# Kernel tuning notes

Measured on AMD Instinct MI355X. Metric: run time of the kernel, lower is better.

The kernel has to match this reference:

```python
import jax, jax.numpy as jnp
import numpy as np

EMB = 64
N_CONS = 100000
N_VARS = 200000
N_EDGES = 2000000


def _embed(x, shift, scale, W1, b1, W2, b2):
    # PreNormLayer (affine) -> Linear -> ReLU -> Linear -> ReLU
    x = (x - shift) * scale
    x = jax.nn.relu(x @ W1 + b1)
    return jax.nn.relu(x @ W2 + b2)


def _biconv(left, right, ei0, ei1, edge_lin, tgt_idx, n_tgt, tgt_feats,
            Wl, bl, Wr, sf, Wf, bf, sp, Woa, boa, Wob, bob):
    # gather-transform: per-edge joint features [E, EMB]
    joint = (left @ Wl + bl)[ei0] + edge_lin + (right @ Wr)[ei1]
    # feature_module_final: PreNorm(scale-only) -> ReLU -> Linear
    msg = jax.nn.relu(joint * sf) @ Wf + bf
    # scatter-add to target nodes, then post-conv PreNorm(scale-only)
    agg = jax.ops.segment_sum(msg, tgt_idx, num_segments=n_tgt) * sp
    h = jax.nn.relu(jnp.concatenate([agg, tgt_feats], axis=1) @ Woa + boa)
    return h @ Wob + bob


def _forward(constraint_features, edge_features, variable_features,
             c_shift, c_scale, c_W1, c_b1, c_W2, c_b2,
             v_shift, v_scale, v_W1, v_b1, v_W2, v_b2,
             e_shift, e_scale,
             vc_Wl, vc_bl, vc_We, vc_Wr, vc_sf, vc_Wf, vc_bf, vc_sp,
             vc_Woa, vc_boa, vc_Wob, vc_bob,
             cv_Wl, cv_bl, cv_We, cv_Wr, cv_sf, cv_Wf, cv_bf, cv_sp,
             cv_Woa, cv_boa, cv_Wob, cv_bob,
             out_W1, out_b1, out_W2, edge_indices):
    ei0, ei1 = edge_indices[0], edge_indices[1]
    c = _embed(constraint_features, c_shift, c_scale, c_W1, c_b1, c_W2, c_b2)
    v = _embed(variable_features, v_shift, v_scale, v_W1, v_b1, v_W2, v_b2)
    e = (edge_features - e_shift) * e_scale  # edge embedding = PreNorm only, dim 1
    # conv_v_to_c (right_to_left=True): target = constraints via ei0
    c = jax.nn.relu(_biconv(c, v, ei0, ei1, e @ vc_We, ei0, N_CONS, c,
                            vc_Wl, vc_bl, vc_Wr, vc_sf, vc_Wf, vc_bf, vc_sp,
                            vc_Woa, vc_boa, vc_Wob, vc_bob))
    # conv_c_to_v: target = variables via ei1
    v = jax.nn.relu(_biconv(c, v, ei0, ei1, e @ cv_We, ei1, N_VARS, v,
                            cv_Wl, cv_bl, cv_Wr, cv_sf, cv_Wf, cv_bf, cv_sp,
                            cv_Woa, cv_boa, cv_Wob, cv_bob))
    out = jax.nn.relu(v @ out_W1 + out_b1) @ out_W2  # [N_VARS, 1]
    return out.reshape(1, -1)


def setup_inputs():
    key = jax.random.key(0)
    ks = iter(jax.random.split(key, 64))

    def rn(shape, s=0.1):
        return (jax.random.normal(next(ks), shape, jnp.float32) * s).astype(jnp.float32)

    d = {}
    d["constraint_features"] = rn((N_CONS, 5), 1.0)
    d["edge_features"] = rn((N_EDGES, 1), 1.0)
    d["variable_features"] = rn((N_VARS, 19), 1.0)

    def prenorm(n, pre):
        d[pre + "shift"] = rn((n,), 0.05)
        d[pre + "scale"] = jnp.ones((n,), jnp.float32) + rn((n,), 0.05)

    prenorm(5, "c_"); prenorm(19, "v_"); prenorm(1, "e_")
    for pre, nin in (("c_", 5), ("v_", 19)):
        d[pre + "W1"] = rn((nin, EMB)); d[pre + "b1"] = rn((EMB,), 0.02)
        d[pre + "W2"] = rn((EMB, EMB)); d[pre + "b2"] = rn((EMB,), 0.02)
    for pre in ("vc_", "cv_"):
        d[pre + "Wl"] = rn((EMB, EMB)); d[pre + "bl"] = rn((EMB,), 0.02)
        d[pre + "We"] = rn((1, EMB)); d[pre + "Wr"] = rn((EMB, EMB))
        d[pre + "sf"] = jnp.float32(1.0) + rn((), 0.05)
        d[pre + "Wf"] = rn((EMB, EMB)); d[pre + "bf"] = rn((EMB,), 0.02)
        d[pre + "sp"] = jnp.float32(1.0) + rn((), 0.05)
        d[pre + "Woa"] = rn((2 * EMB, EMB)); d[pre + "boa"] = rn((EMB,), 0.02)
        d[pre + "Wob"] = rn((EMB, EMB)); d[pre + "bob"] = rn((EMB,), 0.02)
    d["out_W1"] = rn((EMB, EMB)); d["out_b1"] = rn((EMB,), 0.02)
    d["out_W2"] = rn((EMB, 1))
    d["edge_indices"] = jnp.stack([
        jax.random.randint(next(ks), (N_EDGES,), 0, N_CONS),
        jax.random.randint(next(ks), (N_EDGES,), 0, N_VARS)]).astype(jnp.int32)
    d["n_cons_per_sample"] = jnp.array([N_CONS], jnp.int32)
    d["n_vars_per_sample"] = jnp.array([N_VARS], jnp.int32)
    return d


def reference(constraint_features, edge_features, variable_features,
              c_shift, c_scale, c_W1, c_b1, c_W2, c_b2,
              v_shift, v_scale, v_W1, v_b1, v_W2, v_b2,
              e_shift, e_scale,
              vc_Wl, vc_bl, vc_We, vc_Wr, vc_sf, vc_Wf, vc_bf, vc_sp,
              vc_Woa, vc_boa, vc_Wob, vc_bob,
              cv_Wl, cv_bl, cv_We, cv_Wr, cv_sf, cv_Wf, cv_bf, cv_sp,
              cv_Woa, cv_boa, cv_Wob, cv_bob,
              out_W1, out_b1, out_W2,
              edge_indices, n_cons_per_sample, n_vars_per_sample):
    return _forward(constraint_features, edge_features, variable_features,
                    c_shift, c_scale, c_W1, c_b1, c_W2, c_b2,
                    v_shift, v_scale, v_W1, v_b1, v_W2, v_b2,
                    e_shift, e_scale,
                    vc_Wl, vc_bl, vc_We, vc_Wr, vc_sf, vc_Wf, vc_bf, vc_sp,
                    vc_Woa, vc_boa, vc_Wob, vc_bob,
                    cv_Wl, cv_bl, cv_We, cv_Wr, cv_sf, cv_Wf, cv_bf, cv_sp,
                    cv_Woa, cv_boa, cv_Wob, cv_bob,
                    out_W1, out_b1, out_W2, edge_indices)
```

## Files before the change

### kernel.cpp

```cpp
#include <hip/hip_runtime.h>
#include <hip/hip_bf16.h>

#define DEV __device__ __forceinline__

typedef __attribute__((ext_vector_type(8))) short short8;
typedef __attribute__((ext_vector_type(4))) float f32x4;

DEV unsigned short f2bf(float f) {
    __hip_bfloat16 h = __float2bfloat16(f);
    unsigned short u;
    __builtin_memcpy(&u, &h, 2);
    return u;
}
DEV float bf2f(unsigned short u) { return __uint_as_float((unsigned int)u << 16); }

DEV f32x4 mfma_bf16(short8 a, short8 b, f32x4 c) {
    return __builtin_amdgcn_mfma_f32_16x16x32_bf16(a, b, c, 0, 0, 0);
}

DEV void make_hilo(const float* a8, short8& hi, short8& lo) {
    #pragma unroll
    for (int j = 0; j < 8; ++j) {
        const float v = a8[j];
        const unsigned short h = f2bf(v);
        hi[j] = (short)h;
        lo[j] = (short)f2bf(v - bf2f(h));
    }
}

DEV void mfma3(f32x4 acc[4], short8 ah, short8 al,
               const unsigned short* __restrict__ Bh,
               const unsigned short* __restrict__ Bl,
               int nkt, int tidx, int lane) {
    #pragma unroll
    for (int c = 0; c < 4; ++c) {
        const size_t o = ((size_t)(c * nkt + tidx) * 64 + lane) * 8;
        const short8 bh = *(const short8*)(Bh + o);
        const short8 bl = *(const short8*)(Bl + o);
        acc[c] = mfma_bf16(ah, bh, acc[c]);
        acc[c] = mfma_bf16(al, bh, acc[c]);
        acc[c] = mfma_bf16(ah, bl, acc[c]);
    }
}

DEV int swf(int row, int col) {
    return row * 64 + ((((col >> 3) ^ row) & 7) << 3) + (col & 7);
}

DEV void gemm_lds(f32x4 acc[4], const float* Xl,
                  const unsigned short* Bh, const unsigned short* Bl,
                  int nkt, int t0, int ntk, int l15, int q, int lane) {
    for (int t = 0; t < ntk; ++t) {
        const int ch = (t * 4 + q) ^ (l15 & 7);
        const float* a8 = Xl + l15 * 64 + ch * 8;
        short8 ah, al;
        make_hilo(a8, ah, al);
        mfma3(acc, ah, al, Bh, Bl, nkt, t0 + t, lane);
    }
}

DEV void gemm_glb(f32x4 acc[4], const float* __restrict__ Xg, int rbase, int N,
                  const unsigned short* Bh, const unsigned short* Bl,
                  int nkt, int t0, int ntk, int l15, int q, int lane) {
    const int grow = rbase + l15;
    const bool ok = grow < N;
    for (int t = 0; t < ntk; ++t) {
        float a8[8];
        if (ok) {
            const float4 v0 = *(const float4*)(Xg + (size_t)grow * 64 + t * 32 + q * 8);
            const float4 v1 = *(const float4*)(Xg + (size_t)grow * 64 + t * 32 + q * 8 + 4);
            a8[0] = v0.x; a8[1] = v0.y; a8[2] = v0.z; a8[3] = v0.w;
            a8[4] = v1.x; a8[5] = v1.y; a8[6] = v1.z; a8[7] = v1.w;
        } else {
            #pragma unroll
            for (int j = 0; j < 8; ++j) a8[j] = 0.f;
        }
        short8 ah, al;
        make_hilo(a8, ah, al);
        mfma3(acc, ah, al, Bh, Bl, nkt, t0 + t, lane);
    }
}

#define NMAT 15
struct PrepArgs {
    const float* src[NMAT];
    unsigned short* hi[NMAT];
    unsigned short* lo[NMAT];
    int nkt[NMAT];
    int KR[NMAT];
};

__global__ __launch_bounds__(256)
void prep_kernel(PrepArgs pa)
{
    const int m = blockIdx.y;
    const int nkt = pa.nkt[m];
    const int nthr = nkt * 4 * 64;
    const int p = blockIdx.x * 256 + threadIdx.x;
    if (p >= nthr) return;
    const int f = p >> 6, l = p & 63;
    const int c = f / nkt, t = f % nkt;
    const int kbase = t * 32 + ((l >> 4) << 3);
    const int n = c * 16 + (l & 15);
    const float* W = pa.src[m];
    const int KR = pa.KR[m];
    unsigned short* ph = pa.hi[m] + (size_t)p * 8;
    unsigned short* pl = pa.lo[m] + (size_t)p * 8;
    #pragma unroll
    for (int j = 0; j < 8; ++j) {
        const int k = kbase + j;
        const float v = (k < KR) ? W[k * 64 + n] : 0.f;
        const unsigned short h = f2bf(v);
        ph[j] = h;
        pl[j] = f2bf(v - bf2f(h));
    }
}

struct FusedArgs {
    const int* ei; int E; int nH;
    int* h1; int* h2; unsigned int* rank;
    int tC, tV;
    const float* cf; int NC;
    const float* c_shift; const float* c_scale;
    const float* vf; int NV;
    const float* v_shift; const float* v_scale;
    const unsigned short *cW1h, *cW1l, *cW2h, *cW2l, *cWt1h, *cWt1l;
    const unsigned short *vW1h, *vW1l, *vW2h, *vW2l, *vWt1h, *vWt1l, *vWt2h, *vWt2l;
    const float *c_b1, *c_b2, *v_b1, *v_b2, *vc_bl;
    const float *vc_sf, *cv_sf;
    float* Emc; float* Emv;
    unsigned short* A1; unsigned short* B1; unsigned short* B2;
};

__global__ __launch_bounds__(256)
void fused_he_kernel(FusedArgs a)
{
    __shared__ __align__(16) float Bb[4][1024];

    const int half = blockIdx.x & 1;
    const int idx  = blockIdx.x >> 1;

    if (half == 0) {
        const int stride = a.nH * 256;
        for (int e = idx * 256 + (int)threadIdx.x; e < a.E; e += stride) {
            const int r1 = atomicAdd(a.h1 + a.ei[e], 1);
            const int r2 = atomicAdd(a.h2 + a.ei[a.E + e], 1);
            a.rank[e] = (unsigned int)r1 | ((unsigned int)r2 << 16);
        }
        return;
    }

    int tile = idx;
    const float* x; int N; int IN;
    const float *shift, *scale, *b1, *b2, *bt1;
    const unsigned short *W1h, *W1l, *W2h, *W2l, *Wt1h, *Wt1l;
    const unsigned short *Wt2h = nullptr, *Wt2l = nullptr;
    float* Em; unsigned short* T1; unsigned short* T2 = nullptr;
    float sf1, sf2 = 0.f;
    if (tile < a.tC) {
        x = a.cf; N = a.NC; IN = 5; shift = a.c_shift; scale = a.c_scale;
        W1h = a.cW1h; W1l = a.cW1l; b1 = a.c_b1;
        W2h = a.cW2h; W2l = a.cW2l; b2 = a.c_b2;
        Em = a.Emc; Wt1h = a.cWt1h; Wt1l = a.cWt1l; bt1 = a.vc_bl;
        sf1 = a.vc_sf[0]; T1 = a.A1;
    } else {
        tile -= a.tC;
        x = a.vf; N = a.NV; IN = 19; shift = a.v_shift; scale = a.v_scale;
        W1h = a.vW1h; W1l = a.vW1l; b1 = a.v_b1;
        W2h = a.vW2h; W2l = a.vW2l; b2 = a.v_b2;
        Em = a.Emv; Wt1h = a.vWt1h; Wt1l = a.vWt1l; bt1 = nullptr;
        sf1 = a.vc_sf[0]; T1 = a.B1;
        Wt2h = a.vWt2h; Wt2l = a.vWt2l; sf2 = a.cv_sf[0]; T2 = a.B2;
    }

    const int w = threadIdx.x >> 6, lane = threadIdx.x & 63;
    const int l15 = lane & 15, q = lane >> 4;
    const int rbase = tile * 64 + w * 16;

    {
        f32x4 acc[4] = {{0,0,0,0},{0,0,0,0},{0,0,0,0},{0,0,0,0}};
        const int grow = rbase + l15;
        float a8[8];
        #pragma unroll
        for (int j = 0; j < 8; ++j) {
            const int col = q * 8 + j;
            float v = 0.f;
            if (grow < N && col < IN) v = (x[(size_t)grow * IN + col] - shift[col]) * scale[col];
            a8[j] = v;
        }
        short8 ah, al;
        make_hilo(a8, ah, al);
        mfma3(acc, ah, al, W1h, W1l, 1, 0, lane);
        #pragma unroll
        for (int c = 0; c < 4; ++c) {
            const int col = c * 16 + l15;
            const float bb = b1[col];
            #pragma unroll
            for (int r = 0; r < 4; ++r)
                Bb[w][swf(q * 4 + r, col)] = fmaxf(acc[c][r] + bb, 0.f);
        }
    }
    {
        f32x4 acc[4] = {{0,0,0,0},{0,0,0,0},{0,0,0,0},{0,0,0,0}};
        gemm_lds(acc, Bb[w], W2h, W2l, 2, 0, 2, l15, q, lane);
        #pragma unroll
        for (int c = 0; c < 4; ++c) {
            const int col = c * 16 + l15;
            const float bb = b2[col];
            #pragma unroll
            for (int r = 0; r < 4; ++r) {
                const int row = q * 4 + r;
                const int grow = rbase + row;
                const float v = fmaxf(acc[c][r] + bb, 0.f);
                Bb[w][swf(row, col)] = v;
                if (grow < N) Em[(size_t)grow * 64 + col] = v;
            }
        }
    }
    {
        f32x4 acc[4] = {{0,0,0,0},{0,0,0,0},{0,0,0,0},{0,0,0,0}};
        gemm_lds(acc, Bb[w], Wt1h, Wt1l, 2, 0, 2, l15, q, lane);
        #pragma unroll
        for (int c = 0; c < 4; ++c) {
            const int col = c * 16 + l15;
            const float bb = bt1 ? bt1[col] : 0.f;
            #pragma unroll
            for (int r = 0; r < 4; ++r) {
                const int grow = rbase + q * 4 + r;
                if (grow < N) T1[(size_t)grow * 64 + col] = f2bf(sf1 * (acc[c][r] + bb));
            }
        }
    }
    if (T2 != nullptr) {
        f32x4 acc[4] = {{0,0,0,0},{0,0,0,0},{0,0,0,0},{0,0,0,0}};
        gemm_lds(acc, Bb[w], Wt2h, Wt2l, 2, 0, 2, l15, q, lane);
        #pragma unroll
        for (int c = 0; c < 4; ++c) {
            const int col = c * 16 + l15;
            #pragma unroll
            for (int r = 0; r < 4; ++r) {
                const int grow = rbase + q * 4 + r;
                if (grow < N) T2[(size_t)grow * 64 + col] = f2bf(sf2 * acc[c][r]);
            }
        }
    }
}

template<bool IS_POST2>
__global__ __launch_bounds__(256)
void post_mfma(int N, const float* __restrict__ G, const int* __restrict__ rs,
               const float* __restrict__ Em,
               const unsigned short* __restrict__ Wfh, const unsigned short* __restrict__ Wfl,
               const float* __restrict__ bfv, const float* __restrict__ spp,
               const unsigned short* __restrict__ Woah, const unsigned short* __restrict__ Woal,
               const float* __restrict__ boa,
               const unsigned short* __restrict__ Wobh, const unsigned short* __restrict__ Wobl,
               const float* __restrict__ bob,
               const unsigned short* __restrict__ W4h, const unsigned short* __restrict__ W4l,
               const float* __restrict__ b4,
               const float* __restrict__ sf2p, unsigned short* __restrict__ A2,
               const float* __restrict__ oW2, float* __restrict__ out)
{
    __shared__ __align__(16) float BA[4][1024];
    __shared__ __align__(16) float BB[4][1024];

    const int w = threadIdx.x >> 6, lane = threadIdx.x & 63;
    const int l15 = lane & 15, q = lane >> 4;
    const float sp = spp[0];
    const float sf2 = IS_POST2 ? 0.f : sf2p[0];
    const int rbase = blockIdx.x * 64 + w * 16;

    {
        f32x4 acc[4] = {{0,0,0,0},{0,0,0,0},{0,0,0,0},{0,0,0,0}};
        gemm_glb(acc, G, rbase, N, Wfh, Wfl, 2, 0, 2, l15, q, lane);
        float dgr[4];
        #pragma unroll
        for (int r = 0; r < 4; ++r) {
            const int grow = rbase + q * 4 + r;
            dgr[r] = (grow < N) ? (float)(rs[grow + 1] - rs[grow]) : 0.f;
        }
        #pragma unroll
        for (int c = 0; c < 4; ++c) {
            const int col = c * 16 + l15;
            const float bb = bfv[col];
            #pragma unroll
            for (int r = 0; r < 4; ++r)
                BA[w][swf(q * 4 + r, col)] = (acc[c][r] + dgr[r] * bb) * sp;
        }
    }
    {
        f32x4 acc[4] = {{0,0,0,0},{0,0,0,0},{0,0,0,0},{0,0,0,0}};
        gemm_lds(acc, BA[w], Woah, Woal, 4, 0, 2, l15, q, lane);
        gemm_glb(acc, Em, rbase, N, Woah, Woal, 4, 2, 2, l15, q, lane);
        #pragma unroll
        for (int c = 0; c < 4; ++c) {
            const int col = c * 16 + l15;
            const float bb = boa[col];
            #pragma unroll
            for (int r = 0; r < 4; ++r)
                BB[w][swf(q * 4 + r, col)] = fmaxf(acc[c][r] + bb, 0.f);
        }
    }
    {
        f32x4 acc[4] = {{0,0,0,0},{0,0,0,0},{0,0,0,0},{0,0,0,0}};
        gemm_lds(acc, BB[w], Wobh, Wobl, 2, 0, 2, l15, q, lane);
        #pragma unroll
        for (int c = 0; c < 4; ++c) {
            const int col = c * 16 + l15;
            const float bb = bob[col];
            #pragma unroll
            for (int r = 0; r < 4; ++r)
                BA[w][swf(q * 4 + r, col)] = fmaxf(acc[c][r] + bb, 0.f);
        }
    }
    {
        f32x4 acc[4] = {{0,0,0,0},{0,0,0,0},{0,0,0,0},{0,0,0,0}};
        gemm_lds(acc, BA[w], W4h, W4l, 2, 0, 2, l15, q, lane);
        if (!IS_POST2) {
            #pragma unroll
            for (int c = 0; c < 4; ++c) {
                const int col = c * 16 + l15;
                const float bb = b4[col];
                #pragma unroll
                for (int r = 0; r < 4; ++r) {
                    const int grow = rbase + q * 4 + r;
                    if (grow < N) A2[(size_t)grow * 64 + col] = f2bf(sf2 * (acc[c][r] + bb));
                }
            }
        } else {
            float w2c[4], bb4[4];
            #pragma unroll
            for (int c = 0; c < 4; ++c) {
                const int col = c * 16 + l15;
                w2c[c] = oW2[col];
                bb4[c] = b4[col];
            }
            #pragma unroll
            for (int r = 0; r < 4; ++r) {
                float s = 0.f;
                #pragma unroll
                for (int c = 0; c < 4; ++c)
                    s += fmaxf(acc[c][r] + bb4[c], 0.f) * w2c[c];
                s += __shfl_xor(s, 1);
                s += __shfl_xor(s, 2);
                s += __shfl_xor(s, 4);
                s += __shfl_xor(s, 8);
                const int grow = rbase + q * 4 + r;
                if (l15 == 0 && grow < N) out[grow] = s;
            }
        }
    }
}

__global__ __launch_bounds__(256)
void scanA2_kernel(const int* __restrict__ h1, int n1, int* __restrict__ cs1,
                   const int* __restrict__ h2, int n2, int* __restrict__ cs2)
{
    __shared__ int wsum[4];
    const int which = blockIdx.y;
    const int* h = which ? h2 : h1;
    const int n = which ? n2 : n1;
    int* csum = which ? cs2 : cs1;
    if (blockIdx.x * 4096 >= n) return;

    const int t = threadIdx.x, lane = t & 63, wid = t >> 6;
    const int base = blockIdx.x * 4096 + t * 16;
    int s = 0;
    #pragma unroll
    for (int j = 0; j < 16; ++j) {
        const int idx = base + j;
        if (idx < n) s += h[idx];
    }
    #pragma unroll
    for (int d = 1; d < 64; d <<= 1) s += __shfl_xor(s, d);
    if (lane == 0) wsum[wid] = s;
    __syncthreads();
    if (t == 0) csum[blockIdx.x] = wsum[0] + wsum[1] + wsum[2] + wsum[3];
}

__global__ __launch_bounds__(256)
void scanB2_kernel(int* __restrict__ cs1, int nch1, int* __restrict__ rs1, int n1,
                   int* __restrict__ cs2, int nch2, int* __restrict__ rs2, int n2)
{
    __shared__ int wsum[4];
    const int which = blockIdx.x;
    int* csum = which ? cs2 : cs1;
    const int nchunks = which ? nch2 : nch1;
    int* rs = which ? rs2 : rs1;
    const int n = which ? n2 : n1;

    const int t = threadIdx.x, lane = t & 63, wid = t >> 6;
    const int v = (t < nchunks) ? csum[t] : 0;
    int x = v;
    #pragma unroll
    for (int d = 1; d < 64; d <<= 1) { int y = __shfl_up(x, d); if (lane >= d) x += y; }
    if (lane == 63) wsum[wid] = x;
    __syncthreads();
    int woff = 0;
    for (int i = 0; i < wid; ++i) woff += wsum[i];
    if (t < nchunks) csum[t] = woff + x - v;
    if (t == 0) rs[n] = wsum[0] + wsum[1] + wsum[2] + wsum[3];
}

__global__ __launch_bounds__(256)
void scanC2_kernel(const int* __restrict__ h1, int n1, const int* __restrict__ cs1,
                   int* __restrict__ rs1,
                   const int* __restrict__ h2, int n2, const int* __restrict__ cs2,
                   int* __restrict__ rs2)
{
    __shared__ int wsum[4];
    const int which = blockIdx.y;
    const int* h = which ? h2 : h1;
    const int n = which ? n2 : n1;
    const int* csum = which ? cs2 : cs1;
    int* rs = which ? rs2 : rs1;
    if (blockIdx.x * 4096 >= n) return;

    const int t = threadIdx.x, lane = t & 63, wid = t >> 6;
    const int base = blockIdx.x * 4096 + t * 16;
    int loc[16];
    int s = 0;
    #pragma unroll
    for (int j = 0; j < 16; ++j) {
        loc[j] = s;
        const int idx = base + j;
        if (idx < n) s += h[idx];
    }
    int x = s;
    #pragma unroll
    for (int d = 1; d < 64; d <<= 1) { int y = __shfl_up(x, d); if (lane >= d) x += y; }
    if (lane == 63) wsum[wid] = x;
    __syncthreads();
    int woff = 0;
    for (int i = 0; i < wid; ++i) woff += wsum[i];
    const int toff = csum[blockIdx.x] + woff + x - s;
    #pragma unroll
    for (int j = 0; j < 16; ++j) {
        const int idx = base + j;
        if (idx < n) rs[idx] = toff + loc[j];
    }
}

__global__ __launch_bounds__(256)
void scatter_kernel(const int* __restrict__ ei, int E,
                    const float* __restrict__ ef,
                    const float* __restrict__ eshp, const float* __restrict__ escp,
                    const unsigned int* __restrict__ rank,
                    const int* __restrict__ rs1, const int* __restrict__ rs2,
                    int2* __restrict__ pairs1, int2* __restrict__ pairs2)
{
    const int e = blockIdx.x * 256 + threadIdx.x;
    if (e >= E) return;
    const int i0 = ei[e];
    const int i1 = ei[E + e];
    const unsigned int rk = rank[e];
    const float en = (ef[e] - eshp[0]) * escp[0];
    const int enb = __float_as_int(en);
    const int pos1 = rs1[i0] + (int)(rk & 0xffffu);
    const int pos2 = rs2[i1] + (int)(rk >> 16);
    pairs1[pos1] = make_int2(i1, enb);
    pairs2[pos2] = make_int2(i0, enb);
}

DEV void agg_body(int row, int j, const int* __restrict__ rs,
                  const int2* __restrict__ pairs,
                  const unsigned short* __restrict__ Ttgt,
                  const unsigned short* __restrict__ Tsrc,
                  const float* __restrict__ We, const float* __restrict__ sfp,
                  float* __restrict__ G)
{
    const float base = bf2f(Ttgt[(size_t)row * 64 + j]);
    const float sfWe = sfp[0] * We[j];
    const int s = rs[row];
    const int e = rs[row + 1];
    float acc = 0.f;
    int p = s;
    for (; p + 7 < e; p += 8) {
        int2 a[8];
        float b[8];
        #pragma unroll
        for (int u = 0; u < 8; ++u) a[u] = pairs[p + u];
        #pragma unroll
        for (int u = 0; u < 8; ++u) b[u] = bf2f(Tsrc[(size_t)a[u].x * 64 + j]);
        #pragma unroll
        for (int u = 0; u < 8; ++u)
            acc += fmaxf(base + b[u] + __int_as_float(a[u].y) * sfWe, 0.f);
    }
    for (; p < e; ++p) {
        const int2 pr = pairs[p];
        const float bs = bf2f(Tsrc[(size_t)pr.x * 64 + j]);
        acc += fmaxf(base + bs + __int_as_float(pr.y) * sfWe, 0.f);
    }
    G[(size_t)row * 64 + j] = acc;
}

__global__ __launch_bounds__(256)
void agg_kernel(int nrows, const int* __restrict__ rs,
                const int2* __restrict__ pairs,
                const unsigned short* __restrict__ Ttgt,
                const unsigned short* __restrict__ Tsrc,
                const float* __restrict__ We, const float* __restrict__ sfp,
                float* __restrict__ G)
{
    const int row = blockIdx.x * 4 + (int)(threadIdx.x >> 6);
    if (row >= nrows) return;
    agg_body(row, (int)(threadIdx.x & 63), rs, pairs, Ttgt, Tsrc, We, sfp, G);
}

extern "C" void kernel_launch(void* const* d_in, const int* in_sizes, int n_in,
                              void* d_out, int out_size, void* d_ws, size_t ws_size,
                              hipStream_t stream)
{
    const float* cf      = (const float*)d_in[0];
    const float* ef      = (const float*)d_in[1];
    const float* vf      = (const float*)d_in[2];
    const float* c_shift = (const float*)d_in[3];
    const float* c_scale = (const float*)d_in[4];
    const float* v_shift = (const float*)d_in[5];
    const float* v_scale = (const float*)d_in[6];
    const float* e_shift = (const float*)d_in[7];
    const float* e_scale = (const float*)d_in[8];
    const float* c_W1 = (const float*)d_in[9];
    const float* c_b1 = (const float*)d_in[10];
    const float* c_W2 = (const float*)d_in[11];
    const float* c_b2 = (const float*)d_in[12];
    const float* v_W1 = (const float*)d_in[13];
    const float* v_b1 = (const float*)d_in[14];
    const float* v_W2 = (const float*)d_in[15];
    const float* v_b2 = (const float*)d_in[16];
    const float* vc_Wl  = (const float*)d_in[17];
    const float* vc_bl  = (const float*)d_in[18];
    const float* vc_We  = (const float*)d_in[19];
    const float* vc_Wr  = (const float*)d_in[20];
    const float* vc_sf  = (const float*)d_in[21];
    const float* vc_Wf  = (const float*)d_in[22];
    const float* vc_bf  = (const float*)d_in[23];
    const float* vc_sp  = (const float*)d_in[24];
    const float* vc_Woa = (const float*)d_in[25];
    const float* vc_boa = (const float*)d_in[26];
    const float* vc_Wob = (const float*)d_in[27];
    const float* vc_bob = (const float*)d_in[28];
    const float* cv_Wl  = (const float*)d_in[29];
    const float* cv_bl  = (const float*)d_in[30];
    const float* cv_We  = (const float*)d_in[31];
    const float* cv_Wr  = (const float*)d_in[32];
    const float* cv_sf  = (const float*)d_in[33];
    const float* cv_Wf  = (const float*)d_in[34];
    const float* cv_bf  = (const float*)d_in[35];
    const float* cv_sp  = (const float*)d_in[36];
    const float* cv_Woa = (const float*)d_in[37];
    const float* cv_boa = (const float*)d_in[38];
    const float* cv_Wob = (const float*)d_in[39];
    const float* cv_bob = (const float*)d_in[40];
    const float* out_W1 = (const float*)d_in[41];
    const float* out_b1 = (const float*)d_in[42];
    const float* out_W2 = (const float*)d_in[43];
    const int*   eidx   = (const int*)d_in[44];

    const int NC = in_sizes[0] / 5;
    const int NV = in_sizes[2] / 19;
    const int E  = in_sizes[1];

    char* ws = (char*)d_ws;
    size_t off = 0;
    auto alloc = [&](size_t bytes) -> size_t {
        size_t o = off;
        off = (off + bytes + 255) & ~(size_t)255;
        return o;
    };
    size_t o_h1 = alloc((size_t)NC * 4);
    size_t o_h2 = alloc((size_t)NV * 4);
    size_t zero_bytes = off;
    size_t o_rs1  = alloc((size_t)(NC + 1) * 4);
    size_t o_rs2  = alloc((size_t)(NV + 1) * 4);
    size_t o_cs1  = alloc(256 * 4);
    size_t o_cs2  = alloc(256 * 4);
    size_t o_p1   = alloc((size_t)E * 8);
    size_t o_p2   = alloc((size_t)E * 8);
    size_t o_G1   = alloc((size_t)NC * 64 * 4);
    size_t o_G2   = alloc((size_t)NV * 64 * 4);
    size_t o_Emc  = alloc((size_t)NC * 64 * 4);
    size_t o_Emv  = alloc((size_t)NV * 64 * 4);
    size_t o_A1   = alloc((size_t)NC * 64 * 2);
    size_t o_B1   = alloc((size_t)NV * 64 * 2);
    size_t o_B2   = alloc((size_t)NV * 64 * 2);

    static const int nkt_arr[NMAT] = {1,2,2,1,2,2,2,2,4,2,2,2,4,2,2};
    static const int KR_arr[NMAT]  = {5,64,64,19,64,64,64,64,128,64,64,64,128,64,64};
    const float* src_arr[NMAT] = {c_W1, c_W2, vc_Wl, v_W1, v_W2, vc_Wr, cv_Wr,
                                  vc_Wf, vc_Woa, vc_Wob, cv_Wl,
                                  cv_Wf, cv_Woa, cv_Wob, out_W1};
    size_t o_wh[NMAT], o_wl[NMAT];
    for (int m = 0; m < NMAT; ++m) {
        o_wh[m] = alloc((size_t)nkt_arr[m] * 4 * 64 * 8 * 2);
        o_wl[m] = alloc((size_t)nkt_arr[m] * 4 * 64 * 8 * 2);
    }
    (void)ws_size; (void)n_in; (void)out_size;

    int*  h1   = (int*)(ws + o_h1);
    int*  h2   = (int*)(ws + o_h2);
    int*  rs1  = (int*)(ws + o_rs1);
    int*  rs2  = (int*)(ws + o_rs2);
    int*  cs1  = (int*)(ws + o_cs1);
    int*  cs2  = (int*)(ws + o_cs2);
    unsigned int* rank = (unsigned int*)(ws + o_G2);
    int2* p1   = (int2*)(ws + o_p1);
    int2* p2   = (int2*)(ws + o_p2);
    float* G1  = (float*)(ws + o_G1);
    float* G2  = (float*)(ws + o_G2);
    float* Emc = (float*)(ws + o_Emc);
    float* Emv = (float*)(ws + o_Emv);
    unsigned short* A1 = (unsigned short*)(ws + o_A1);
    unsigned short* B1 = (unsigned short*)(ws + o_B1);
    unsigned short* A2 = (unsigned short*)(ws + o_A1);
    unsigned short* B2 = (unsigned short*)(ws + o_B2);

    PrepArgs pa;
    for (int m = 0; m < NMAT; ++m) {
        pa.src[m] = src_arr[m];
        pa.hi[m] = (unsigned short*)(ws + o_wh[m]);
        pa.lo[m] = (unsigned short*)(ws + o_wl[m]);
        pa.nkt[m] = nkt_arr[m];
        pa.KR[m] = KR_arr[m];
    }
    auto WH = [&](int m) { return (const unsigned short*)(ws + o_wh[m]); };
    auto WL = [&](int m) { return (const unsigned short*)(ws + o_wl[m]); };

    hipMemsetAsync(ws, 0, zero_bytes, stream);

    prep_kernel<<<dim3(4, NMAT), 256, 0, stream>>>(pa);

    const int tC = (NC + 63) >> 6, tV = (NV + 63) >> 6;
    const int nE = tC + tV;
    FusedArgs fa;
    fa.ei = eidx; fa.E = E; fa.nH = nE;
    fa.h1 = h1; fa.h2 = h2; fa.rank = rank;
    fa.tC = tC; fa.tV = tV;
    fa.cf = cf; fa.NC = NC; fa.c_shift = c_shift; fa.c_scale = c_scale;
    fa.vf = vf; fa.NV = NV; fa.v_shift = v_shift; fa.v_scale = v_scale;
    fa.cW1h = WH(0); fa.cW1l = WL(0); fa.cW2h = WH(1); fa.cW2l = WL(1);
    fa.cWt1h = WH(2); fa.cWt1l = WL(2);
    fa.vW1h = WH(3); fa.vW1l = WL(3); fa.vW2h = WH(4); fa.vW2l = WL(4);
    fa.vWt1h = WH(5); fa.vWt1l = WL(5); fa.vWt2h = WH(6); fa.vWt2l = WL(6);
    fa.c_b1 = c_b1; fa.c_b2 = c_b2; fa.v_b1 = v_b1; fa.v_b2 = v_b2;
    fa.vc_bl = vc_bl; fa.vc_sf = vc_sf; fa.cv_sf = cv_sf;
    fa.Emc = Emc; fa.Emv = Emv; fa.A1 = A1; fa.B1 = B1; fa.B2 = B2;
    fused_he_kernel<<<2 * nE, 256, 0, stream>>>(fa);

    const int nch1 = (NC + 4095) / 4096, nch2 = (NV + 4095) / 4096;
    const int nchm = nch1 > nch2 ? nch1 : nch2;
    scanA2_kernel<<<dim3(nchm, 2), 256, 0, stream>>>(h1, NC, cs1, h2, NV, cs2);
    scanB2_kernel<<<2, 256, 0, stream>>>(cs1, nch1, rs1, NC, cs2, nch2, rs2, NV);
    scanC2_kernel<<<dim3(nchm, 2), 256, 0, stream>>>(h1, NC, cs1, rs1, h2, NV, cs2, rs2);

    scatter_kernel<<<(E + 255) / 256, 256, 0, stream>>>(
        eidx, E, ef, e_shift, e_scale, rank, rs1, rs2, p1, p2);

    agg_kernel<<<(NC + 3) / 4, 256, 0, stream>>>(
        NC, rs1, p1, A1, B1, vc_We, vc_sf, G1);
    post_mfma<false><<<tC, 256, 0, stream>>>(
        NC, G1, rs1, Emc,
        WH(7), WL(7), vc_bf, vc_sp,
        WH(8), WL(8), vc_boa,
        WH(9), WL(9), vc_bob,
        WH(10), WL(10), cv_bl,
        cv_sf, A2, nullptr, nullptr);

    agg_kernel<<<(NV + 3) / 4, 256, 0, stream>>>(
        NV, rs2, p2, B2, A2, cv_We, cv_sf, G2);
    post_mfma<true><<<tV, 256, 0, stream>>>(
        NV, G2, rs2, Emv,
        WH(11), WL(11), cv_bf, cv_sp,
        WH(12), WL(12), cv_boa,
        WH(13), WL(13), cv_bob,
        WH(14), WL(14), out_b1,
        nullptr, nullptr, out_W2, (float*)d_out);
}
```

Measured before the change: 724.3 us.

## Privatize degree histograms per XCD to keep atomics within the local L2

The edge-degree histogram now keeps eight copies, one per XCD. Each block reads its XCD id from a hardware register and counts into its own copy with relaxed, workgroup-scoped atomics, so the atomics can resolve in the local L2 instead of as device-wide atomics. The XCD id is packed into the top bits of each 16-bit rank. The scan kernels sum the eight copies and write per-XCD base offsets, which the scatter kernel uses to place each edge. The cost is larger memset and scan traffic, a 13-bit cap on per-XCD degree, and reliance on workgroup-scope atomics staying correct across blocks that share an XCD.

```diff
diff --git a/kernel.cpp b/kernel.cpp
--- a/kernel.cpp
+++ b/kernel.cpp
@@ -141,11 +141,20 @@
     const int idx  = blockIdx.x >> 1;
 
     if (half == 0) {
+        int xcd;
+        asm volatile("s_getreg_b32 %0, hwreg(HW_REG_XCC_ID)" : "=s"(xcd));
+        xcd &= 7;
+        int* h1x = a.h1 + (size_t)xcd * a.NC;
+        int* h2x = a.h2 + (size_t)xcd * a.NV;
+        const unsigned int xtag = (unsigned int)xcd << 13;
         const int stride = a.nH * 256;
         for (int e = idx * 256 + (int)threadIdx.x; e < a.E; e += stride) {
-            const int r1 = atomicAdd(a.h1 + a.ei[e], 1);
-            const int r2 = atomicAdd(a.h2 + a.ei[a.E + e], 1);
-            a.rank[e] = (unsigned int)r1 | ((unsigned int)r2 << 16);
+            const int r1 = __hip_atomic_fetch_add(h1x + a.ei[e], 1,
+                              __ATOMIC_RELAXED, __HIP_MEMORY_SCOPE_WORKGROUP);
+            const int r2 = __hip_atomic_fetch_add(h2x + a.ei[a.E + e], 1,
+                              __ATOMIC_RELAXED, __HIP_MEMORY_SCOPE_WORKGROUP);
+            a.rank[e] = ((unsigned int)r1 | xtag) |
+                        ((((unsigned int)r2) | xtag) << 16);
         }
         return;
     }
@@ -369,7 +378,10 @@
     #pragma unroll
     for (int j = 0; j < 16; ++j) {
         const int idx = base + j;
-        if (idx < n) s += h[idx];
+        if (idx < n) {
+            #pragma unroll
+            for (int xs = 0; xs < 8; ++xs) s += h[(size_t)xs * n + idx];
+        }
     }
     #pragma unroll
     for (int d = 1; d < 64; d <<= 1) s += __shfl_xor(s, d);
@@ -404,9 +416,9 @@
 
 __global__ __launch_bounds__(256)
 void scanC2_kernel(const int* __restrict__ h1, int n1, const int* __restrict__ cs1,
-                   int* __restrict__ rs1,
+                   int* __restrict__ rs1, int* __restrict__ b1,
                    const int* __restrict__ h2, int n2, const int* __restrict__ cs2,
-                   int* __restrict__ rs2)
+                   int* __restrict__ rs2, int* __restrict__ b2)
 {
     __shared__ int wsum[4];
     const int which = blockIdx.y;
@@ -414,6 +426,7 @@
     const int n = which ? n2 : n1;
     const int* csum = which ? cs2 : cs1;
     int* rs = which ? rs2 : rs1;
+    int* bs = which ? b2 : b1;
     if (blockIdx.x * 4096 >= n) return;
 
     const int t = threadIdx.x, lane = t & 63, wid = t >> 6;
@@ -424,7 +437,12 @@
     for (int j = 0; j < 16; ++j) {
         loc[j] = s;
         const int idx = base + j;
-        if (idx < n) s += h[idx];
+        if (idx < n) {
+            int tt = 0;
+            #pragma unroll
+            for (int xs = 0; xs < 8; ++xs) tt += h[(size_t)xs * n + idx];
+            s += tt;
+        }
     }
     int x = s;
     #pragma unroll
@@ -437,7 +455,15 @@
     #pragma unroll
     for (int j = 0; j < 16; ++j) {
         const int idx = base + j;
-        if (idx < n) rs[idx] = toff + loc[j];
+        if (idx < n) {
+            int c = toff + loc[j];
+            rs[idx] = c;
+            #pragma unroll
+            for (int xs = 0; xs < 8; ++xs) {
+                bs[(size_t)xs * n + idx] = c;
+                c += h[(size_t)xs * n + idx];
+            }
+        }
     }
 }
 
@@ -446,7 +472,8 @@
                     const float* __restrict__ ef,
                     const float* __restrict__ eshp, const float* __restrict__ escp,
                     const unsigned int* __restrict__ rank,
-                    const int* __restrict__ rs1, const int* __restrict__ rs2,
+                    const int* __restrict__ b1s, const int* __restrict__ b2s,
+                    int NC, int NV,
                     int2* __restrict__ pairs1, int2* __restrict__ pairs2)
 {
     const int e = blockIdx.x * 256 + threadIdx.x;
@@ -456,8 +483,10 @@
     const unsigned int rk = rank[e];
     const float en = (ef[e] - eshp[0]) * escp[0];
     const int enb = __float_as_int(en);
-    const int pos1 = rs1[i0] + (int)(rk & 0xffffu);
-    const int pos2 = rs2[i1] + (int)(rk >> 16);
+    const unsigned int rk1 = rk & 0xffffu;
+    const unsigned int rk2 = rk >> 16;
+    const int pos1 = b1s[(size_t)(rk1 >> 13) * NC + i0] + (int)(rk1 & 0x1fffu);
+    const int pos2 = b2s[(size_t)(rk2 >> 13) * NV + i1] + (int)(rk2 & 0x1fffu);
     pairs1[pos1] = make_int2(i1, enb);
     pairs2[pos2] = make_int2(i0, enb);
 }
@@ -568,9 +597,6 @@
         off = (off + bytes + 255) & ~(size_t)255;
         return o;
     };
-    size_t o_h1 = alloc((size_t)NC * 4);
-    size_t o_h2 = alloc((size_t)NV * 4);
-    size_t zero_bytes = off;
     size_t o_rs1  = alloc((size_t)(NC + 1) * 4);
     size_t o_rs2  = alloc((size_t)(NV + 1) * 4);
     size_t o_cs1  = alloc(256 * 4);
@@ -597,8 +623,10 @@
     }
     (void)ws_size; (void)n_in; (void)out_size;
 
-    int*  h1   = (int*)(ws + o_h1);
-    int*  h2   = (int*)(ws + o_h2);
+    int*  h1s  = (int*)(ws + o_p1);
+    int*  h2s  = (int*)(ws + o_p1 + (size_t)8 * NC * 4);
+    int*  b1s  = (int*)(ws + o_G1);
+    int*  b2s  = (int*)(ws + o_G1 + (size_t)8 * NC * 4);
     int*  rs1  = (int*)(ws + o_rs1);
     int*  rs2  = (int*)(ws + o_rs2);
     int*  cs1  = (int*)(ws + o_cs1);
@@ -626,7 +654,7 @@
     auto WH = [&](int m) { return (const unsigned short*)(ws + o_wh[m]); };
     auto WL = [&](int m) { return (const unsigned short*)(ws + o_wl[m]); };
 
-    hipMemsetAsync(ws, 0, zero_bytes, stream);
+    hipMemsetAsync(ws + o_p1, 0, (size_t)8 * (NC + NV) * 4, stream);
 
     prep_kernel<<<dim3(4, NMAT), 256, 0, stream>>>(pa);
 
@@ -634,7 +662,7 @@
     const int nE = tC + tV;
     FusedArgs fa;
     fa.ei = eidx; fa.E = E; fa.nH = nE;
-    fa.h1 = h1; fa.h2 = h2; fa.rank = rank;
+    fa.h1 = h1s; fa.h2 = h2s; fa.rank = rank;
     fa.tC = tC; fa.tV = tV;
     fa.cf = cf; fa.NC = NC; fa.c_shift = c_shift; fa.c_scale = c_scale;
     fa.vf = vf; fa.NV = NV; fa.v_shift = v_shift; fa.v_scale = v_scale;
@@ -649,12 +677,13 @@
 
     const int nch1 = (NC + 4095) / 4096, nch2 = (NV + 4095) / 4096;
     const int nchm = nch1 > nch2 ? nch1 : nch2;
-    scanA2_kernel<<<dim3(nchm, 2), 256, 0, stream>>>(h1, NC, cs1, h2, NV, cs2);
+    scanA2_kernel<<<dim3(nchm, 2), 256, 0, stream>>>(h1s, NC, cs1, h2s, NV, cs2);
     scanB2_kernel<<<2, 256, 0, stream>>>(cs1, nch1, rs1, NC, cs2, nch2, rs2, NV);
-    scanC2_kernel<<<dim3(nchm, 2), 256, 0, stream>>>(h1, NC, cs1, rs1, h2, NV, cs2, rs2);
+    scanC2_kernel<<<dim3(nchm, 2), 256, 0, stream>>>(
+        h1s, NC, cs1, rs1, b1s, h2s, NV, cs2, rs2, b2s);
 
     scatter_kernel<<<(E + 255) / 256, 256, 0, stream>>>(
-        eidx, E, ef, e_shift, e_scale, rank, rs1, rs2, p1, p2);
+        eidx, E, ef, e_shift, e_scale, rank, b1s, b2s, NC, NV, p1, p2);
 
     agg_kernel<<<(NC + 3) / 4, 256, 0, stream>>>(
         NC, rs1, p1, A1, B1, vc_We, vc_sf, G1);
```

New measurement: 778.7 us. 7.5% more time.

## Replace global-atomic edge histogram with sliced LDS-windowed histogram

Applied to the files above, without the earlier changes.

Edge degree counting and per-edge ranks move out of global atomics. A separate histogram kernel splits edges into slices and node ranges into 16K-entry LDS windows, counts with shared-memory atomics, and writes per-slice partial histograms plus 16-bit local ranks. An offset-sum kernel turns the partials into per-slice offsets and totals, and the scatter kernel adds those offsets. Each window block rereads its slice of edge indices, which multiplies index reads by the window count, and embedding is no longer fused with the histogram.

```diff
diff --git a/kernel.cpp b/kernel.cpp
--- a/kernel.cpp
+++ b/kernel.cpp
@@ -5,6 +5,9 @@
 
 typedef __attribute__((ext_vector_type(8))) short short8;
 typedef __attribute__((ext_vector_type(4))) float f32x4;
+
+#define HWIN 16384
+#define NSLICE 32
 
 DEV unsigned short f2bf(float f) {
     __hip_bfloat16 h = __float2bfloat16(f);
@@ -116,9 +119,72 @@
     }
 }
 
-struct FusedArgs {
-    const int* ei; int E; int nH;
-    int* h1; int* h2; unsigned int* rank;
+__global__ __launch_bounds__(256)
+void hist_kernel(const int* __restrict__ ei, int E, int slice_len, int nW1,
+                 int NP1, int NP2,
+                 int* __restrict__ Hp1, int* __restrict__ Hp2,
+                 unsigned short* __restrict__ rl1, unsigned short* __restrict__ rl2)
+{
+    __shared__ int lh[HWIN];
+    const int s = blockIdx.x;
+    const int w = blockIdx.y;
+    const int d2 = (w >= nW1) ? 1 : 0;
+    const int wl = d2 ? (w - nW1) : w;
+    const int lo = wl * HWIN;
+    const int* __restrict__ key = d2 ? (ei + E) : ei;
+    unsigned short* __restrict__ rl = d2 ? rl2 : rl1;
+    int* __restrict__ Hp = d2 ? (Hp2 + (size_t)s * NP2) : (Hp1 + (size_t)s * NP1);
+
+    for (int i = threadIdx.x; i < HWIN; i += 256) lh[i] = 0;
+    __syncthreads();
+
+    const int e0 = s * slice_len;
+    const int e1 = (e0 + slice_len < E) ? (e0 + slice_len) : E;
+    const int tid = threadIdx.x;
+    const int nv4 = (e1 - e0) >> 2;
+    for (int g = tid; g < nv4; g += 256) {
+        const int e4 = e0 + g * 4;
+        const int4 kk = *(const int4*)(key + e4);
+        const int ks[4] = {kk.x, kk.y, kk.z, kk.w};
+        #pragma unroll
+        for (int u = 0; u < 4; ++u) {
+            const unsigned int d = (unsigned int)(ks[u] - lo);
+            if (d < HWIN)
+                rl[e4 + u] = (unsigned short)atomicAdd(&lh[d], 1);
+        }
+    }
+    for (int e = e0 + (nv4 << 2) + tid; e < e1; e += 256) {
+        const unsigned int d = (unsigned int)(key[e] - lo);
+        if (d < HWIN)
+            rl[e] = (unsigned short)atomicAdd(&lh[d], 1);
+    }
+    __syncthreads();
+    for (int i = threadIdx.x; i < HWIN; i += 256) Hp[lo + i] = lh[i];
+}
+
+__global__ __launch_bounds__(256)
+void offsum_kernel(int NP1, int* __restrict__ Hp1, int* __restrict__ h1, int n1,
+                   int NP2, int* __restrict__ Hp2, int* __restrict__ h2, int n2)
+{
+    const int which = blockIdx.y;
+    int* __restrict__ Hp = which ? Hp2 : Hp1;
+    int* __restrict__ h = which ? h2 : h1;
+    const int n = which ? n2 : n1;
+    const int NP = which ? NP2 : NP1;
+    const int k = blockIdx.x * 256 + (int)threadIdx.x;
+    if (k >= n) return;
+    int run = 0;
+    #pragma unroll
+    for (int s = 0; s < NSLICE; ++s) {
+        int* p = Hp + (size_t)s * NP + k;
+        const int t = *p;
+        *p = run;
+        run += t;
+    }
+    h[k] = run;
+}
+
+struct EmbedArgs {
     int tC, tV;
     const float* cf; int NC;
     const float* c_shift; const float* c_scale;
@@ -133,24 +199,11 @@
 };
 
 __global__ __launch_bounds__(256)
-void fused_he_kernel(FusedArgs a)
+void embed_kernel(EmbedArgs a)
 {
     __shared__ __align__(16) float Bb[4][1024];
 
-    const int half = blockIdx.x & 1;
-    const int idx  = blockIdx.x >> 1;
-
-    if (half == 0) {
-        const int stride = a.nH * 256;
-        for (int e = idx * 256 + (int)threadIdx.x; e < a.E; e += stride) {
-            const int r1 = atomicAdd(a.h1 + a.ei[e], 1);
-            const int r2 = atomicAdd(a.h2 + a.ei[a.E + e], 1);
-            a.rank[e] = (unsigned int)r1 | ((unsigned int)r2 << 16);
-        }
-        return;
-    }
-
-    int tile = idx;
+    int tile = blockIdx.x;
     const float* x; int N; int IN;
     const float *shift, *scale, *b1, *b2, *bt1;
     const unsigned short *W1h, *W1l, *W2h, *W2l, *Wt1h, *Wt1l;
@@ -442,22 +495,25 @@
 }
 
 __global__ __launch_bounds__(256)
-void scatter_kernel(const int* __restrict__ ei, int E,
+void scatter_kernel(const int* __restrict__ ei, int E, int slice_len,
                     const float* __restrict__ ef,
                     const float* __restrict__ eshp, const float* __restrict__ escp,
-                    const unsigned int* __restrict__ rank,
+                    const unsigned short* __restrict__ rl1,
+                    const unsigned short* __restrict__ rl2,
+                    const int* __restrict__ off1, int NP1,
+                    const int* __restrict__ off2, int NP2,
                     const int* __restrict__ rs1, const int* __restrict__ rs2,
                     int2* __restrict__ pairs1, int2* __restrict__ pairs2)
 {
-    const int e = blockIdx.x * 256 + threadIdx.x;
+    const int e = blockIdx.x * 256 + (int)threadIdx.x;
     if (e >= E) return;
+    const int s = e / slice_len;
     const int i0 = ei[e];
     const int i1 = ei[E + e];
-    const unsigned int rk = rank[e];
     const float en = (ef[e] - eshp[0]) * escp[0];
     const int enb = __float_as_int(en);
-    const int pos1 = rs1[i0] + (int)(rk & 0xffffu);
-    const int pos2 = rs2[i1] + (int)(rk >> 16);
+    const int pos1 = rs1[i0] + off1[(size_t)s * NP1 + i0] + (int)rl1[e];
+    const int pos2 = rs2[i1] + off2[(size_t)s * NP2 + i1] + (int)rl2[e];
     pairs1[pos1] = make_int2(i1, enb);
     pairs2[pos2] = make_int2(i0, enb);
 }
@@ -561,6 +617,12 @@
     const int NV = in_sizes[2] / 19;
     const int E  = in_sizes[1];
 
+    const int nW1 = (NC + HWIN - 1) / HWIN;
+    const int nW2 = (NV + HWIN - 1) / HWIN;
+    const int NP1 = nW1 * HWIN;
+    const int NP2 = nW2 * HWIN;
+    const int slice_len = (((E + NSLICE - 1) / NSLICE) + 3) & ~3;
+
     char* ws = (char*)d_ws;
     size_t off = 0;
     auto alloc = [&](size_t bytes) -> size_t {
@@ -568,9 +630,8 @@
         off = (off + bytes + 255) & ~(size_t)255;
         return o;
     };
-    size_t o_h1 = alloc((size_t)NC * 4);
-    size_t o_h2 = alloc((size_t)NV * 4);
-    size_t zero_bytes = off;
+    auto r256 = [](size_t x) -> size_t { return (x + 255) & ~(size_t)255; };
+
     size_t o_rs1  = alloc((size_t)(NC + 1) * 4);
     size_t o_rs2  = alloc((size_t)(NV + 1) * 4);
     size_t o_cs1  = alloc(256 * 4);
@@ -597,13 +658,23 @@
     }
     (void)ws_size; (void)n_in; (void)out_size;
 
+    size_t o_rl1 = o_G1;
+    size_t o_rl2 = o_rl1 + r256((size_t)E * 2);
+    size_t o_h1  = o_rl2 + r256((size_t)E * 2);
+    size_t o_h2  = o_h1  + r256((size_t)NC * 4);
+    size_t o_Hp1 = o_G2;
+    size_t o_Hp2 = o_Hp1 + r256((size_t)NSLICE * NP1 * 4);
+
+    unsigned short* rl1 = (unsigned short*)(ws + o_rl1);
+    unsigned short* rl2 = (unsigned short*)(ws + o_rl2);
     int*  h1   = (int*)(ws + o_h1);
     int*  h2   = (int*)(ws + o_h2);
+    int*  Hp1  = (int*)(ws + o_Hp1);
+    int*  Hp2  = (int*)(ws + o_Hp2);
     int*  rs1  = (int*)(ws + o_rs1);
     int*  rs2  = (int*)(ws + o_rs2);
     int*  cs1  = (int*)(ws + o_cs1);
     int*  cs2  = (int*)(ws + o_cs2);
-    unsigned int* rank = (unsigned int*)(ws + o_G2);
     int2* p1   = (int2*)(ws + o_p1);
     int2* p2   = (int2*)(ws + o_p2);
     float* G1  = (float*)(ws + o_G1);
@@ -626,26 +697,12 @@
     auto WH = [&](int m) { return (const unsigned short*)(ws + o_wh[m]); };
     auto WL = [&](int m) { return (const unsigned short*)(ws + o_wl[m]); };
 
-    hipMemsetAsync(ws, 0, zero_bytes, stream);
-
     prep_kernel<<<dim3(4, NMAT), 256, 0, stream>>>(pa);
 
-    const int tC = (NC + 63) >> 6, tV = (NV + 63) >> 6;
-    const int nE = tC + tV;
-    FusedArgs fa;
-    fa.ei = eidx; fa.E = E; fa.nH = nE;
-    fa.h1 = h1; fa.h2 = h2; fa.rank = rank;
-    fa.tC = tC; fa.tV = tV;
-    fa.cf = cf; fa.NC = NC; fa.c_shift = c_shift; fa.c_scale = c_scale;
-    fa.vf = vf; fa.NV = NV; fa.v_shift = v_shift; fa.v_scale = v_scale;
-    fa.cW1h = WH(0); fa.cW1l = WL(0); fa.cW2h = WH(1); fa.cW2l = WL(1);
-    fa.cWt1h = WH(2); fa.cWt1l = WL(2);
-    fa.vW1h = WH(3); fa.vW1l = WL(3); fa.vW2h = WH(4); fa.vW2l = WL(4);
-    fa.vWt1h = WH(5); fa.vWt1l = WL(5); fa.vWt2h = WH(6); fa.vWt2l = WL(6);
-    fa.c_b1 = c_b1; fa.c_b2 = c_b2; fa.v_b1 = v_b1; fa.v_b2 = v_b2;
-    fa.vc_bl = vc_bl; fa.vc_sf = vc_sf; fa.cv_sf = cv_sf;
-    fa.Emc = Emc; fa.Emv = Emv; fa.A1 = A1; fa.B1 = B1; fa.B2 = B2;
-    fused_he_kernel<<<2 * nE, 256, 0, stream>>>(fa);
+    hist_kernel<<<dim3(NSLICE, nW1 + nW2), 256, 0, stream>>>(
+        eidx, E, slice_len, nW1, NP1, NP2, Hp1, Hp2, rl1, rl2);
+    offsum_kernel<<<dim3((((NC > NV) ? NC : NV) + 255) / 256, 2), 256, 0, stream>>>(
+        NP1, Hp1, h1, NC, NP2, Hp2, h2, NV);
 
     const int nch1 = (NC + 4095) / 4096, nch2 = (NV + 4095) / 4096;
     const int nchm = nch1 > nch2 ? nch1 : nch2;
@@ -653,8 +710,24 @@
     scanB2_kernel<<<2, 256, 0, stream>>>(cs1, nch1, rs1, NC, cs2, nch2, rs2, NV);
     scanC2_kernel<<<dim3(nchm, 2), 256, 0, stream>>>(h1, NC, cs1, rs1, h2, NV, cs2, rs2);
 
+    const int tC = (NC + 63) >> 6, tV = (NV + 63) >> 6;
+    const int nE = tC + tV;
+    EmbedArgs ea;
+    ea.tC = tC; ea.tV = tV;
+    ea.cf = cf; ea.NC = NC; ea.c_shift = c_shift; ea.c_scale = c_scale;
+    ea.vf = vf; ea.NV = NV; ea.v_shift = v_shift; ea.v_scale = v_scale;
+    ea.cW1h = WH(0); ea.cW1l = WL(0); ea.cW2h = WH(1); ea.cW2l = WL(1);
+    ea.cWt1h = WH(2); ea.cWt1l = WL(2);
+    ea.vW1h = WH(3); ea.vW1l = WL(3); ea.vW2h = WH(4); ea.vW2l = WL(4);
+    ea.vWt1h = WH(5); ea.vWt1l = WL(5); ea.vWt2h = WH(6); ea.vWt2l = WL(6);
+    ea.c_b1 = c_b1; ea.c_b2 = c_b2; ea.v_b1 = v_b1; ea.v_b2 = v_b2;
+    ea.vc_bl = vc_bl; ea.vc_sf = vc_sf; ea.cv_sf = cv_sf;
+    ea.Emc = Emc; ea.Emv = Emv; ea.A1 = A1; ea.B1 = B1; ea.B2 = B2;
+    embed_kernel<<<nE, 256, 0, stream>>>(ea);
+
     scatter_kernel<<<(E + 255) / 256, 256, 0, stream>>>(
-        eidx, E, ef, e_shift, e_scale, rank, rs1, rs2, p1, p2);
+        eidx, E, slice_len, ef, e_shift, e_scale,
+        rl1, rl2, Hp1, NP1, Hp2, NP2, rs1, rs2, p1, p2);
 
     agg_kernel<<<(NC + 3) / 4, 256, 0, stream>>>(
         NC, rs1, p1, A1, B1, vc_We, vc_sf, G1);
```

Result: slower. 755.0 us (+4.2%).
